# Optimization experiments

Hardware: AMD Instinct MI355X
Metric: run time of the kernel (lower is better)

The kernel has to match this reference:

```python
import jax, jax.numpy as jnp
import numpy as np
from jax import lax

H = 32      # n_heads
D = 128     # head_dim
HID = 4096  # hidden_dim
CQ, CK, CH = 4, 9, 2
G = H // CH  # conv groups == groupnorm groups == 16


def setup_inputs() -> dict:
    key = jax.random.key(0)
    ks = jax.random.split(key, 8)
    q_seqlen = np.array([512, 384, 384, 256], dtype=np.int64)
    kv_seqlen = np.array([512, 384, 384, 256], dtype=np.int64)
    Sq = int(q_seqlen.sum())
    Sk = int(kv_seqlen.sum())
    x = jax.random.normal(ks[0], (Sq, HID), dtype=jnp.float32) * 0.02
    context = jax.random.normal(ks[1], (Sk, HID), dtype=jnp.float32) * 0.02
    wq = jax.random.normal(ks[2], (HID, H * D), dtype=jnp.float32) * 0.02
    wkv = jax.random.normal(ks[3], (HID, 2 * H * D), dtype=jnp.float32) * 0.02
    wo = jax.random.normal(ks[4], (H * D, HID), dtype=jnp.float32) * 0.02
    # grouped conv kernel [out=H, in_per_group=CH, CQ, CK]; dirac-like identity + noise
    conv_w = jax.random.normal(ks[5], (H, CH, CQ, CK), dtype=jnp.float32) * 0.05
    conv_w = conv_w.at[jnp.arange(H), jnp.arange(H) % CH, CQ // 2, CK // 2].add(1.0)
    gn_w = jnp.ones((H,), dtype=jnp.float32)
    gn_b = jnp.zeros((H,), dtype=jnp.float32)
    return {"x": x, "context": context, "wq": wq, "wkv": wkv, "wo": wo,
            "conv_w": conv_w, "gn_w": gn_w, "gn_b": gn_b,
            "q_seqlen": q_seqlen, "kv_seqlen": kv_seqlen}


def _block_diag_mask(q_seqlen, kv_seqlen, dtype):
    # block-diagonal ones mask for packed ragged sequences (static lengths)
    q_len = np.asarray(q_seqlen)
    k_len = np.asarray(kv_seqlen)
    seg_q = np.repeat(np.arange(len(q_len)), q_len)
    seg_k = np.repeat(np.arange(len(k_len)), k_len)
    return jnp.asarray(seg_q[:, None] == seg_k[None, :], dtype=dtype)


def reference(x, context, wq, wkv, wo, conv_w, gn_w, gn_b, q_seqlen, kv_seqlen):
    S = x.shape[0]
    mask = _block_diag_mask(q_seqlen, kv_seqlen, x.dtype)  # [Sq, Sk]
    scale = 1.0 / np.sqrt(D).astype(np.float32)
    q = (x @ wq).reshape(S, H, D).transpose(1, 0, 2) * scale        # [H, Sq, D]
    kv = context @ wkv
    k = kv[:, : H * D].reshape(-1, H, D).transpose(1, 0, 2)         # [H, Sk, D]
    v = kv[:, H * D :].reshape(-1, H, D).transpose(1, 0, 2)         # [H, Sk, D]
    attn = jnp.einsum('hqd,hkd->hqk', q, k) * mask[None]            # [H, Sq, Sk]
    # grouped Conv2d over (query, key) positions, channels = heads
    a = lax.conv_general_dilated(
        attn[None], conv_w, window_strides=(1, 1),
        padding=((CQ // 2, CQ // 2), (CK // 2, CK // 2)),
        dimension_numbers=('NCHW', 'OIHW', 'NCHW'),
        feature_group_count=G)[0]                                   # [H, Sq+1, Sk]
    a = a[:, :-1, :]  # c_q even -> drop extra row (c_k odd -> no col drop)
    a = jax.nn.softmax(a + mask[None], axis=-1)                     # note: +1 bias inside blocks, not -inf
    out = jnp.einsum('hqk,hkd->hqd', a, v)                          # [H, Sq, D]
    # GroupNorm(num_groups=G, channels=H) over [1, H, Sq, D]
    og = out.reshape(G, CH, S, D)
    mu = og.mean(axis=(1, 2, 3), keepdims=True)
    var = og.var(axis=(1, 2, 3), keepdims=True)
    og = (og - mu) * lax.rsqrt(var + 1e-5)
    out = og.reshape(H, S, D) * gn_w[:, None, None] + gn_b[:, None, None]
    out = out.transpose(1, 0, 2).reshape(S, H * D)
    return out @ wo
```

## Files before the change

kernel.cpp:

```cpp
#include <hip/hip_runtime.h>
#include <stdint.h>


#define H_   32
#define D_   128
#define HID_ 4096
#define WMAX2 944
#define LPAD 8

typedef unsigned short bfr;
typedef __attribute__((ext_vector_type(4))) float f32x4;
typedef __attribute__((ext_vector_type(4))) int   i32x4;
typedef __attribute__((ext_vector_type(8))) unsigned short u16x8;
typedef __attribute__((ext_vector_type(4))) unsigned short u16x4;

__device__ __forceinline__ bfr f2bf(float f) {
  uint32_t u = __float_as_uint(f);
  u += 0x7fffu + ((u >> 16) & 1u);
  return (bfr)(u >> 16);
}
__device__ __forceinline__ float bf2f(bfr u) {
  return __uint_as_float(((uint32_t)u) << 16);
}
__device__ __forceinline__ void mfma_bf16(f32x4& d, i32x4 a, i32x4 b) {
// ... 63 lines not shown

__global__ __launch_bounds__(256) void transpose_cvt(
    const float* __restrict__ in, bfr* __restrict__ out, int R, int ld)
{
  __shared__ float tile[64][65];
  const int t = threadIdx.x;
  const int rb = blockIdx.y * 64, cb = blockIdx.x * 64;
  const int row = t >> 2, c4 = (t & 3) * 16;
  const float* gp = in + (long long)(rb + row) * ld + cb + c4;
  #pragma unroll
  for (int j = 0; j < 4; ++j) {
    f32x4 v = *(const f32x4*)(gp + j * 4);
    #pragma unroll
    for (int q = 0; q < 4; ++q) tile[row][c4 + j * 4 + q] = v[q];
  }
  __syncthreads();
  const int cc = row, r4 = c4;
  u16x8 a, b;
  #pragma unroll
  for (int j = 0; j < 8; ++j) a[j] = f2bf(tile[r4 + j][cc]);
  #pragma unroll
  for (int j = 0; j < 8; ++j) b[j] = f2bf(tile[r4 + 8 + j][cc]);
  bfr* op = out + (long long)(cb + cc) * R + rb + r4;
  *(u16x8*)op = a;
  *(u16x8*)(op + 8) = b;
}

__global__ __launch_bounds__(256) void transpose_b16(
    const bfr* __restrict__ in, bfr* __restrict__ out, int R, int C)
{
  __shared__ bfr t[64][72];
  const int z = blockIdx.z;
  const bfr* ip = in + (long long)z * R * C;
  bfr* op = out + (long long)z * R * C;
  const int rb = blockIdx.y * 64, cb = blockIdx.x * 64;
  const int tr = threadIdx.x >> 3;
  const int tc = (threadIdx.x & 7) * 8;
  #pragma unroll
  for (int half = 0; half < 2; ++half) {
    const int r = tr + half * 32;
    u16x8 v = *(const u16x8*)(ip + (long long)(rb + r) * C + cb + tc);
    *(u16x8*)&t[r][tc] = v;
  }
  __syncthreads();
  #pragma unroll
  for (int half = 0; half < 2; ++half) {
    const int cc = tr + half * 32;
    u16x8 vv;
    #pragma unroll
    for (int j = 0; j < 8; ++j) vv[j] = t[tc + j][cc];
    *(u16x8*)(op + (long long)(cb + cc) * R + rb + tc) = vv;
  }
}

__global__ __launch_bounds__(256) void colsum_v(
    const bfr* __restrict__ vt, float* __restrict__ cs, int Sk)
{
  const int lane = threadIdx.x & 63, wave = threadIdx.x >> 6;
  const int row = blockIdx.x * 4 + wave;
  const bfr* src = vt + (long long)row * Sk;
  float s = 0.f;
  for (int i = lane * 8; i + 8 <= Sk; i += 512) {
    u16x8 v = *(const u16x8*)(src + i);
    #pragma unroll
    for (int j = 0; j < 8; ++j) s += bf2f(v[j]);
  }
  #pragma unroll
  for (int m = 1; m < 64; m <<= 1) s += __shfl_xor(s, m);
  if (lane == 0) cs[row] = s;
}

struct GemmAux {
  const int* segq; const int* segk; const int* bk;
  bfr* qb; bfr* kb; bfr* vrow;
  float* outb; float* stats;
  const float* fvArr; const float* colsum;
  float scale;
  int S, Sk, nOff;
};

enum { MODE_PLAIN = 0, MODE_Q = 1, MODE_KV = 2, MODE_QK = 3, MODE_PV = 4 };

template <int MODE, int KS = 1>
__global__ __launch_bounds__(256) void gemm_bt(
    const bfr* __restrict__ A, const bfr* __restrict__ Bt, void* __restrict__ Cout,
    int N, int K, int lda, int ldb,
    long long aZ, long long bZ, long long cZ, GemmAux aux)
{
  __shared__ bfr As[128 * 32];
  __shared__ bfr Bs[128 * 32];
  __shared__ float redS[8], redSS[8];
  const int tid = threadIdx.x;
  const int lane = tid & 63;
  const int wave = tid >> 6;
  const int z = blockIdx.z;

  int bx = blockIdx.x, by = blockIdx.y;
  {
    const int gx = gridDim.x, gy = gridDim.y;
    if (((gx & 3) == 0) && ((gy & 1) == 0)) {
      const int lid = by * gx + bx;
      const int xcd = lid & 7, inner = lid >> 3;
      const int cm = gy >> 1, cn = gx >> 2;
      by = (xcd >> 2) * cm + inner / cn;
      bx = (xcd & 3) * cn + inner % cn;
    }
  }
  const int m0 = by * 128;
  const int n0 = bx * 128;
  const bfr* Ap = A + (long long)z * aZ;
  const bfr* Bp = Bt + (long long)z * bZ;

  if constexpr (MODE == MODE_QK) {
    const int t127 = min(m0 + 127, aux.S - 1);
    const int loT = max(aux.bk[aux.segq[max(m0 - 2, 0)]] - 4, 0);
    const int hiT = min(aux.bk[aux.segq[min(t127 + 1, aux.S - 1)] + 1] + 4, aux.Sk);
    if (n0 > hiT + 16 || n0 + 127 < loT - 16) return;
    const int sm0 = aux.segq[m0], sm1 = aux.segq[t127];
    const int sn0 = aux.segk[n0], sn1 = aux.segk[min(n0 + 127, aux.Sk - 1)];
    if (sm1 < sn0 || sn1 < sm0) {
      bfr* C = (bfr*)Cout + (long long)z * cZ + (long long)m0 * aux.Sk + n0;
      const i32x4 zz = {0, 0, 0, 0};
      #pragma unroll
      for (int c = 0; c < 8; ++c) {
        int id = c * 256 + tid;
        int r = id >> 4, col = (id & 15) * 8;
        *(i32x4*)(C + (long long)r * aux.Sk + col) = zz;
      }
      return;
    }
  }

  int kLo = 0, kHiV = K;
  if constexpr (KS > 1) {
    const int kspan = K / KS;
    kLo = z * kspan;
    kHiV = kLo + kspan;
  }
  if constexpr (MODE == MODE_PV) {
    const int t127 = min(m0 + 127, aux.S - 1);
    kLo = (max(aux.bk[aux.segq[max(m0 - 2, 0)]] - 4, 0)) & ~31;
    int th = min(aux.bk[aux.segq[min(t127 + 1, aux.S - 1)] + 1] + 4, aux.Sk);
    kHiV = min((th + 31) & ~31, aux.Sk);
  }

  const int wr = (wave >> 1) * 64;
  const int wc = (wave & 1) * 64;
  f32x4 acc[4][4];
  #pragma unroll
  for (int i = 0; i < 4; ++i)
    #pragma unroll
    for (int j = 0; j < 4; ++j) acc[i][j] = (f32x4){0.f, 0.f, 0.f, 0.f};

  const int srow = lane >> 2;
  const int scol = (((lane & 3) ^ ((lane >> 2) & 3)) << 3);
  const int rcol = (((lane >> 4) ^ (lane & 3)) << 3);

  const int kSteps = (kHiV - kLo) >> 5;
  for (int ks = 0; ks < kSteps; ++ks) {
    const int k0 = kLo + (ks << 5);
    #pragma unroll
    for (int c = 0; c < 4; ++c) {
      const int chunk = (wave << 2) + c;
      const int ci = chunk & 7;
      const int row = ci * 16 + srow;
      if (chunk < 8) gload_lds16(Ap + (long long)(m0 + row) * lda + k0 + scol, As + ci * 512);
      else           gload_lds16(Bp + (long long)(n0 + row) * ldb + k0 + scol, Bs + ci * 512);
    }
    __syncthreads();
    i32x4 af[4], bfv[4];
    #pragma unroll
    for (int i = 0; i < 4; ++i)
      af[i] = *(const i32x4*)&As[(wr + i * 16 + (lane & 15)) * 32 + rcol];
    #pragma unroll
    for (int i = 0; i < 4; ++i)
      bfv[i] = *(const i32x4*)&Bs[(wc + i * 16 + (lane & 15)) * 32 + rcol];
    #pragma unroll
    for (int i = 0; i < 4; ++i)
      #pragma unroll
      for (int j = 0; j < 4; ++j)
        mfma_bf16(acc[i][j], af[i], bfv[j]);
    __syncthreads();
  }

  bool qkUni = false;
  int sgm[16], sgn[4];
  float fvm[16], csn[4];
  if constexpr (MODE == MODE_QK) {
    const int sA = aux.segq[m0], sB = aux.segq[min(m0 + 127, aux.S - 1)];
    const int sC = aux.segk[n0], sD = aux.segk[min(n0 + 127, aux.Sk - 1)];
    qkUni = (sA == sB) && (sC == sD);
    if (!qkUni) {
      #pragma unroll
      for (int i = 0; i < 4; ++i)
        #pragma unroll
        for (int r = 0; r < 4; ++r)
          sgm[i * 4 + r] = aux.segq[m0 + wr + i * 16 + (lane >> 4) * 4 + r];
      #pragma unroll
      for (int j = 0; j < 4; ++j) sgn[j] = aux.segk[n0 + wc + j * 16 + (lane & 15)];
    }
  }
  if constexpr (MODE == MODE_PV) {
    #pragma unroll
    for (int i = 0; i < 4; ++i)
      #pragma unroll
      for (int r = 0; r < 4; ++r)
        fvm[i * 4 + r] = aux.fvArr[(long long)z * aux.S + m0 + wr + i * 16 + (lane >> 4) * 4 + r];
    #pragma unroll
    for (int j = 0; j < 4; ++j)
      csn[j] = aux.colsum[(long long)z * D_ + n0 + wc + j * 16 + (lane & 15)];
  }

  float sv = 0.f, sq2 = 0.f;
  #pragma unroll
  for (int i = 0; i < 4; ++i) {
    #pragma unroll
    for (int j = 0; j < 4; ++j) {
      #pragma unroll
      for (int r = 0; r < 4; ++r) {
        const int m = m0 + wr + i * 16 + (lane >> 4) * 4 + r;
        const int n = n0 + wc + j * 16 + (lane & 15);
        const float v = acc[i][j][r];
        if constexpr (KS > 1) {
          aux.outb[((long long)z * aux.S + m) * N + n] = v;
        } else if constexpr (MODE == MODE_PLAIN) {
          ((float*)Cout)[(long long)m * N + n] = v;
        } else if constexpr (MODE == MODE_Q) {
          const int hh = n >> 7, d = n & 127;
          aux.qb[((long long)hh * aux.S + m) * D_ + d] = f2bf(v * aux.scale);
        } else if constexpr (MODE == MODE_KV) {
          const int ng = n + aux.nOff;
          if (ng < H_ * D_) {
            const int hh = ng >> 7, d = ng & 127;
            aux.kb[((long long)hh * aux.Sk + m) * D_ + d] = f2bf(v);
          } else {
            const int nv = ng - H_ * D_;
            const int hh = nv >> 7, d = nv & 127;
            aux.vrow[((long long)hh * aux.Sk + m) * D_ + d] = f2bf(v);
          }
        } else if constexpr (MODE == MODE_QK) {
          const float vv = (qkUni || sgm[i * 4 + r] == sgn[j]) ? v : 0.f;
          ((bfr*)Cout)[(long long)z * cZ + (long long)m * aux.Sk + n] = f2bf(vv);
        } else if constexpr (MODE == MODE_PV) {
          const float vv = v + fvm[i * 4 + r] * csn[j];
          aux.outb[((long long)z * aux.S + m) * D_ + n] = vv;
          sv += vv; sq2 += vv * vv;
        }
      }
    }
  }

  if constexpr (MODE == MODE_PV && KS == 1) {
    #pragma unroll
    for (int msk = 1; msk < 64; msk <<= 1) {
      sv  += __shfl_xor(sv, msk);
      sq2 += __shfl_xor(sq2, msk);
    }
    if (lane == 0) { redS[wave] = sv; redSS[wave] = sq2; }
    __syncthreads();
    if (tid == 0) {
      const float a = redS[0] + redS[1] + redS[2] + redS[3];
      const float b = redSS[0] + redSS[1] + redSS[2] + redSS[3];
      atomicAdd(&aux.stats[(z >> 1) * 2 + 0], a);
      atomicAdd(&aux.stats[(z >> 1) * 2 + 1], b);
    }
  }
}

__global__ __launch_bounds__(256) void reduce_split_q(
    const float* __restrict__ part, bfr* __restrict__ qb, float scale, int S)
{
  const long long MN = (long long)S * HID_;
  const long long i = ((long long)blockIdx.x * 256 + threadIdx.x) * 8;
  if (i >= MN) return;
  const f32x4 a0 = *(const f32x4*)(part + i);
  const f32x4 a1 = *(const f32x4*)(part + i + 4);
  const f32x4 b0 = *(const f32x4*)(part + MN + i);
  const f32x4 b1 = *(const f32x4*)(part + MN + i + 4);
  const int m = (int)(i >> 12);
  const int n = (int)(i & 4095);
  const int hh = n >> 7, d = n & 127;
  u16x8 o;
  #pragma unroll
  for (int j = 0; j < 4; ++j) {
    o[j]     = f2bf((a0[j] + b0[j]) * scale);
    o[4 + j] = f2bf((a1[j] + b1[j]) * scale);
  }
  *(u16x8*)(qb + ((long long)hh * S + m) * D_ + d) = o;
}

__global__ __launch_bounds__(256) void reduce_split_f32(
    const float* __restrict__ part, float* __restrict__ out, long long MN)
{
  const long long i = ((long long)blockIdx.x * 256 + threadIdx.x) * 8;
  if (i >= MN) return;
  const f32x4 a0 = *(const f32x4*)(part + i);
  const f32x4 a1 = *(const f32x4*)(part + i + 4);
  const f32x4 b0 = *(const f32x4*)(part + MN + i);
  const f32x4 b1 = *(const f32x4*)(part + MN + i + 4);
  f32x4 o0, o1;
  #pragma unroll
  for (int j = 0; j < 4; ++j) { o0[j] = a0[j] + b0[j]; o1[j] = a1[j] + b1[j]; }
  *(f32x4*)(out + i) = o0;
  *(f32x4*)(out + i + 4) = o1;
}

__global__ __launch_bounds__(256) void conv_softmax4(
    const bfr* __restrict__ attn, const float* __restrict__ conv_w,
    bfr* __restrict__ p, float* __restrict__ fvArr,
    const int* __restrict__ segq, const int* __restrict__ segk,
    const int* __restrict__ bk, int S, int Sk, int h0)
{
  __shared__ float wsh[144];
  __shared__ bfr sIn[7][WMAX2];
  const int tid = threadIdx.x, lane = tid & 63, w = tid >> 6;
  const int q0 = blockIdx.x * 4;
  const int c0 = blockIdx.y * 2;
  const int h  = h0 + c0;
  if (tid < 144) wsh[tid] = conv_w[h * 72 + tid];

  const int lo0 = (max(bk[segq[max(q0 - 2, 0)]] - 4, 0)) & ~7;
  const int hiL = min(bk[segq[min(q0 + 4, S - 1)] + 1] + 4, Sk);
  const int g0 = max(lo0 - 8, 0) & ~7;
  const int g1 = min(hiL + 4, Sk);
  const int W8 = (g1 - g0 + 7) >> 3;

  const int qa = q0 + w;
  const int loA = (max(bk[segq[max(qa - 2, 0)]] - 4, 0)) & ~7;
  const int hiA = min(bk[segq[min(qa + 1, S - 1)] + 1] + 4, Sk);
  const int sqA = segq[qa];
  const int width = hiA - loA;

  float lg[2][4][4];
  #pragma unroll
  for (int e = 0; e < 2; ++e)
    #pragma unroll
    for (int pp = 0; pp < 4; ++pp)
      #pragma unroll
      for (int o = 0; o < 4; ++o) lg[e][pp][o] = 0.f;

  if (tid < 7) {
    const u16x8 zz8 = {0,0,0,0,0,0,0,0};
    *(u16x8*)&sIn[tid][0] = zz8;
    *(u16x8*)&sIn[tid][LPAD + W8 * 8] = zz8;
  }

  for (int pass = 0; pass < 2; ++pass) {
    if (pass) __syncthreads();
    const bfr* src0 = attn + (long long)(c0 + pass) * S * Sk;
    for (int it = tid; it < 7 * 116; it += 256) {
      const int ri = it / 116;
      const int j  = it - ri * 116;
      if (j < W8) {
        const int r = q0 - 2 + ri;
        u16x8 v = {0,0,0,0,0,0,0,0};
        if (r >= 0 && r < S) v = *(const u16x8*)(src0 + (long long)r * Sk + g0 + j * 8);
        *(u16x8*)&sIn[ri][LPAD + j * 8] = v;
      }
    }
    __syncthreads();

    #pragma unroll
    for (int pp = 0; pp < 4; ++pp) {
      const int kk = loA + pp * 256 + lane * 4;
      if (kk < hiA) {
        const int ib = LPAD + kk - 4 - g0;
        #pragma unroll
        for (int rr = 0; rr < 4; ++rr) {
          const bfr* sp = &sIn[w + rr][ib];
          u16x4 u0 = *(const u16x4*)(sp);
          u16x4 u1 = *(const u16x4*)(sp + 4);
          u16x4 u2 = *(const u16x4*)(sp + 8);
          float xx[12];
          #pragma unroll
          for (int j2 = 0; j2 < 4; ++j2) {
            xx[j2]     = bf2f(u0[j2]);
            xx[4 + j2] = bf2f(u1[j2]);
            xx[8 + j2] = bf2f(u2[j2]);
          }
          const float* wv0 = &wsh[(pass * 4 + rr) * 9];
          const float* wv1 = wv0 + 72;
          #pragma unroll
          for (int dk = 0; dk < 9; ++dk) {
            #pragma unroll
            for (int o = 0; o < 4; ++o) {
              lg[0][pp][o] += xx[o + dk] * wv0[dk];
              lg[1][pp][o] += xx[o + dk] * wv1[dk];
            }
          }
        }
      }
    }
  }

  float lmax0 = -1e30f, lmax1 = -1e30f;
  #pragma unroll
  for (int pp = 0; pp < 4; ++pp) {
    const int kk = loA + pp * 256 + lane * 4;
    i32x4 sk4 = {0, 0, 0, 0};
    if (kk < Sk) sk4 = *(const i32x4*)&segk[kk];
    #pragma unroll
    for (int o = 0; o < 4; ++o) {
      const int k = kk + o;
      float v0 = -1e30f, v1 = -1e30f;
      if (k < hiA) {
        const float mb = (sk4[o] == sqA) ? 1.f : 0.f;
        v0 = lg[0][pp][o] + mb; lmax0 = fmaxf(lmax0, v0);
        v1 = lg[1][pp][o] + mb; lmax1 = fmaxf(lmax1, v1);
      }
      lg[0][pp][o] = v0; lg[1][pp][o] = v1;
    }
  }
  #pragma unroll
  for (int m = 1; m < 64; m <<= 1) {
    lmax0 = fmaxf(lmax0, __shfl_xor(lmax0, m));
    lmax1 = fmaxf(lmax1, __shfl_xor(lmax1, m));
  }
  const float M0 = fmaxf(lmax0, 0.f), M1 = fmaxf(lmax1, 0.f);
  float ls0 = 0.f, ls1 = 0.f;
  #pragma unroll
  for (int pp = 0; pp < 4; ++pp)
    #pragma unroll
    for (int o = 0; o < 4; ++o) {
      const float e0 = __expf(lg[0][pp][o] - M0);
      const float e1 = __expf(lg[1][pp][o] - M1);
      lg[0][pp][o] = e0; ls0 += e0;
      lg[1][pp][o] = e1; ls1 += e1;
    }
  #pragma unroll
  for (int m = 1; m < 64; m <<= 1) {
    ls0 += __shfl_xor(ls0, m);
    ls1 += __shfl_xor(ls1, m);
  }
// ... 80 lines not shown
                              void* d_out, int out_size, void* d_ws, size_t ws_size,
                              hipStream_t stream)
{
  const float* x      = (const float*)d_in[0];
  const float* ctx    = (const float*)d_in[1];
  const float* wq     = (const float*)d_in[2];
  const float* wkv    = (const float*)d_in[3];
  const float* wo     = (const float*)d_in[4];
  const float* conv_w = (const float*)d_in[5];
  const float* gnw    = (const float*)d_in[6];
  const float* gnb    = (const float*)d_in[7];
  const void*  qsl    = d_in[8];
  const void*  ksl    = d_in[9];
  const int S    = in_sizes[0] / HID_;
  const int Sk   = in_sizes[1] / HID_;
  const int nseg = in_sizes[8];

  auto al = [](size_t v) { return (v + 255) & ~(size_t)255; };
  char* base = (char*)d_ws;
  size_t off = 0;
  auto take = [&](size_t bytes) -> char* { char* r = base + off; off += al(bytes); return r; };

  int*   segq  = (int*)take((size_t)S * 4);
  int*   segk  = (int*)take((size_t)Sk * 4);
  int*   bq    = (int*)take(64);
  int*   bk    = (int*)take(64);
  float* stats = (float*)take(128);
  float* mr    = (float*)take(128);
  float* fvArr = (float*)take((size_t)H_ * S * 4);
  float* csV   = (float*)take((size_t)H_ * D_ * 4);
  bfr*   qb    = (bfr*)take((size_t)H_ * S * D_ * 2);
  bfr*   kbuf  = (bfr*)take((size_t)H_ * Sk * D_ * 2);
  bfr*   vrow  = (bfr*)take((size_t)H_ * Sk * D_ * 2);
  bfr*   vt    = (bfr*)take((size_t)H_ * Sk * D_ * 2);
  float* outb  = (float*)take((size_t)H_ * S * D_ * 4);
  const size_t poolBase = off;
  char*  pool  = base + poolBase;

  const int Smax = (S > Sk) ? S : Sk;
  const size_t A1 = al((size_t)Smax * HID_ * 2);
  const size_t WT = al((size_t)HID_ * HID_ * 2);
  const size_t PART = al((size_t)2 * S * HID_ * 4);

  const size_t CAmin = al((size_t)4 * S * Sk * 2);
  const size_t fusedNeed = (A1 + 2 * WT > 2 * CAmin) ? (A1 + 2 * WT) : (2 * CAmin);
  const bool fused = (poolBase + fusedNeed <= ws_size);
  const bool splitOK = (poolBase + A1 + 2 * WT + PART <= ws_size);
  const size_t wNeed = A1 + (fused ? 2 : 1) * WT + (splitOK ? PART : 0);

  int nc = 4;
  {
    const int cands[3] = {32, 16, 8};
    for (int ci = 0; ci < 3; ++ci) {
      const size_t CA = al((size_t)cands[ci] * S * Sk * 2);
      const size_t need = (wNeed > 2 * CA) ? wNeed : (2 * CA);
      if (poolBase + need <= ws_size) { nc = cands[ci]; break; }
    }
  }
  const size_t CA = al((size_t)nc * S * Sk * 2);
  bfr*   xcb    = (bfr*)pool;
  bfr*   wT     = (bfr*)(pool + A1);
  float* partB  = (float*)(pool + A1 + 2 * WT);
  bfr*   attn_c = (bfr*)pool;
  bfr*   pbuf_c = (bfr*)(pool + CA);

  seg_setup<<<1, 256, 0, stream>>>(qsl, ksl, segq, segk, bq, bk, stats, S, Sk, nseg);

  GemmAux aux{};
  aux.segq = segq; aux.segk = segk; aux.bk = bk;
  aux.qb = qb; aux.kb = kbuf; aux.vrow = vrow;
  aux.outb = outb; aux.stats = stats;
  aux.fvArr = fvArr; aux.colsum = csV;
  aux.scale = 0.08838834764831845f;
  aux.S = S; aux.Sk = Sk; aux.nOff = 0;

  const long long MN = (long long)S * HID_;
  const int nRed = (int)((MN / 8 + 255) / 256);

  const long long nx = (long long)S * HID_;
  cvt_bf16<<<(int)((nx / 8 + 255) / 256), 256, 0, stream>>>(x, xcb, nx);
  transpose_cvt<<<dim3(HID_ / 64, HID_ / 64), 256, 0, stream>>>(wq, wT, HID_, HID_);
  if (splitOK) {
    GemmAux auxQ = aux; auxQ.outb = partB;
    gemm_bt<MODE_Q, 2><<<dim3(HID_ / 128, S / 128, 2), 256, 0, stream>>>(
        xcb, wT, nullptr, HID_, HID_, HID_, HID_, 0, 0, 0, auxQ);
    reduce_split_q<<<nRed, 256, 0, stream>>>(partB, qb, aux.scale, S);
  } else {
    gemm_bt<MODE_Q><<<dim3(HID_ / 128, S / 128, 1), 256, 0, stream>>>(
        xcb, wT, nullptr, HID_, HID_, HID_, HID_, 0, 0, 0, aux);
  }

  const long long nctx = (long long)Sk * HID_;
  cvt_bf16<<<(int)((nctx / 8 + 255) / 256), 256, 0, stream>>>(ctx, xcb, nctx);
  if (fused) {
    transpose_cvt<<<dim3(2 * HID_ / 64, HID_ / 64), 256, 0, stream>>>(wkv, wT, HID_, 2 * HID_);
    gemm_bt<MODE_KV><<<dim3(2 * HID_ / 128, Sk / 128, 1), 256, 0, stream>>>(
        xcb, wT, nullptr, 2 * HID_, HID_, HID_, HID_, 0, 0, 0, aux);
  } else {
    transpose_cvt<<<dim3(HID_ / 64, HID_ / 64), 256, 0, stream>>>(wkv, wT, HID_, 2 * HID_);
    gemm_bt<MODE_KV><<<dim3(HID_ / 128, Sk / 128, 1), 256, 0, stream>>>(
        xcb, wT, nullptr, HID_, HID_, HID_, HID_, 0, 0, 0, aux);
    transpose_cvt<<<dim3(HID_ / 64, HID_ / 64), 256, 0, stream>>>(wkv + HID_, wT, HID_, 2 * HID_);
    GemmAux auxV = aux; auxV.nOff = H_ * D_;
    gemm_bt<MODE_KV><<<dim3(HID_ / 128, Sk / 128, 1), 256, 0, stream>>>(
        xcb, wT, nullptr, HID_, HID_, HID_, HID_, 0, 0, 0, auxV);
  }

  transpose_b16<<<dim3(D_ / 64, Sk / 64, H_), 256, 0, stream>>>(vrow, vt, Sk, D_);
  colsum_v<<<H_ * D_ / 4, 256, 0, stream>>>(vt, csV, Sk);

  for (int h0 = 0; h0 < H_; h0 += nc) {
    gemm_bt<MODE_QK><<<dim3(Sk / 128, S / 128, nc), 256, 0, stream>>>(
        qb + (size_t)h0 * S * D_, kbuf + (size_t)h0 * Sk * D_, attn_c,
        Sk, D_, D_, D_,
        (long long)S * D_, (long long)Sk * D_, (long long)S * Sk, aux);
    conv_softmax4<<<dim3(S / 4, nc / 2), 256, 0, stream>>>(
        attn_c, conv_w, pbuf_c, fvArr, segq, segk, bk, S, Sk, h0);
    GemmAux auxP = aux;
    auxP.outb = outb + (size_t)h0 * S * D_;
    auxP.stats = stats + h0;
    auxP.fvArr = fvArr + (size_t)h0 * S;
    auxP.colsum = csV + (size_t)h0 * D_;
    gemm_bt<MODE_PV><<<dim3(1, S / 128, nc), 256, 0, stream>>>(
        pbuf_c, vt + (size_t)h0 * D_ * Sk, nullptr,
        D_, Sk, Sk, Sk,
        (long long)S * Sk, (long long)D_ * Sk, 0, auxP);
  }

  gn_finalize<<<1, 32, 0, stream>>>(stats, mr, 1.0f / (2.0f * S * D_));
  gn_apply<<<dim3((S * D_) / 2048, H_), 256, 0, stream>>>(outb, mr, gnw, gnb, xcb, S);
  transpose_cvt<<<dim3(HID_ / 64, HID_ / 64), 256, 0, stream>>>(wo, wT, HID_, HID_);
  if (splitOK) {
    GemmAux auxO = aux; auxO.outb = partB;
    gemm_bt<MODE_PLAIN, 2><<<dim3(HID_ / 128, S / 128, 2), 256, 0, stream>>>(
        xcb, wT, nullptr, HID_, HID_, HID_, HID_, 0, 0, 0, auxO);
    reduce_split_f32<<<nRed, 256, 0, stream>>>(partB, (float*)d_out, MN);
  } else {
    gemm_bt<MODE_PLAIN><<<dim3(HID_ / 128, S / 128, 1), 256, 0, stream>>>(
        xcb, wT, d_out, HID_, HID_, HID_, HID_, 0, 0, 0, aux);
  }
}
```

Baseline: 544.0 us.

## Add double-buffered 512-thread GEMM for projections and widen conv-softmax blocks

Adds a new gemm_bt8 kernel with 8 waves, a BK=64 tile and double-buffered LDS staging. It prefetches the next k-tile with async global-to-LDS loads while MFMAs run on the current one, and is used for the Q, KV and output projection GEMMs. The QK/PV GEMM keeps the old kernel but loses its XOR swizzle, which may bring back LDS bank conflicts. The conv-softmax kernel now processes 8 query rows per 512-thread block instead of 4, reusing more of the staged halo rows. The larger LDS footprint (64KB for the GEMM) lowers occupancy.

```diff
diff --git a/kernel.cpp b/kernel.cpp
--- a/kernel.cpp
+++ b/kernel.cpp
@@ -169,14 +169,12 @@
 enum { MODE_PLAIN = 0, MODE_Q = 1, MODE_KV = 2, MODE_QK = 3, MODE_PV = 4 };
 
 template <int MODE, int KS = 1>
-__global__ __launch_bounds__(256) void gemm_bt(
+__global__ __launch_bounds__(512) void gemm_bt8(
     const bfr* __restrict__ A, const bfr* __restrict__ Bt, void* __restrict__ Cout,
-    int N, int K, int lda, int ldb,
-    long long aZ, long long bZ, long long cZ, GemmAux aux)
-{
-  __shared__ bfr As[128 * 32];
-  __shared__ bfr Bs[128 * 32];
-  __shared__ float redS[8], redSS[8];
+    int N, int K, int lda, int ldb, GemmAux aux)
+{
+  __shared__ bfr As[2][128 * 64];
+  __shared__ bfr Bs[2][128 * 64];
   const int tid = threadIdx.x;
   const int lane = tid & 63;
   const int wave = tid >> 6;
@@ -193,116 +191,69 @@
       bx = (xcd & 3) * cn + inner % cn;
     }
   }
-  const int m0 = by * 128;
-  const int n0 = bx * 128;
-  const bfr* Ap = A + (long long)z * aZ;
-  const bfr* Bp = Bt + (long long)z * bZ;
-
-  if constexpr (MODE == MODE_QK) {
-    const int t127 = min(m0 + 127, aux.S - 1);
-    const int loT = max(aux.bk[aux.segq[max(m0 - 2, 0)]] - 4, 0);
-    const int hiT = min(aux.bk[aux.segq[min(t127 + 1, aux.S - 1)] + 1] + 4, aux.Sk);
-    if (n0 > hiT + 16 || n0 + 127 < loT - 16) return;
-    const int sm0 = aux.segq[m0], sm1 = aux.segq[t127];
-    const int sn0 = aux.segk[n0], sn1 = aux.segk[min(n0 + 127, aux.Sk - 1)];
-    if (sm1 < sn0 || sn1 < sm0) {
-      bfr* C = (bfr*)Cout + (long long)z * cZ + (long long)m0 * aux.Sk + n0;
-      const i32x4 zz = {0, 0, 0, 0};
-      #pragma unroll
-      for (int c = 0; c < 8; ++c) {
-        int id = c * 256 + tid;
-        int r = id >> 4, col = (id & 15) * 8;
-        *(i32x4*)(C + (long long)r * aux.Sk + col) = zz;
-      }
-      return;
-    }
-  }
-
-  int kLo = 0, kHiV = K;
-  if constexpr (KS > 1) {
-    const int kspan = K / KS;
-    kLo = z * kspan;
-    kHiV = kLo + kspan;
-  }
-  if constexpr (MODE == MODE_PV) {
-    const int t127 = min(m0 + 127, aux.S - 1);
-    kLo = (max(aux.bk[aux.segq[max(m0 - 2, 0)]] - 4, 0)) & ~31;
-    int th = min(aux.bk[aux.segq[min(t127 + 1, aux.S - 1)] + 1] + 4, aux.Sk);
-    kHiV = min((th + 31) & ~31, aux.Sk);
-  }
-
-  const int wr = (wave >> 1) * 64;
-  const int wc = (wave & 1) * 64;
-  f32x4 acc[4][4];
+  const int m0 = by * 128, n0 = bx * 128;
+
+  int kLo = 0, kHi = K;
+  if constexpr (KS > 1) { const int ksp = K / KS; kLo = z * ksp; kHi = kLo + ksp; }
+
+  const int wr = (wave >> 2) * 64;
+  const int wc = (wave & 3) * 32;
+  f32x4 acc[4][2];
   #pragma unroll
   for (int i = 0; i < 4; ++i)
     #pragma unroll
-    for (int j = 0; j < 4; ++j) acc[i][j] = (f32x4){0.f, 0.f, 0.f, 0.f};
-
-  const int srow = lane >> 2;
-  const int scol = (((lane & 3) ^ ((lane >> 2) & 3)) << 3);
-  const int rcol = (((lane >> 4) ^ (lane & 3)) << 3);
-
-  const int kSteps = (kHiV - kLo) >> 5;
-  for (int ks = 0; ks < kSteps; ++ks) {
-    const int k0 = kLo + (ks << 5);
+    for (int j = 0; j < 2; ++j) acc[i][j] = (f32x4){0.f, 0.f, 0.f, 0.f};
+
+  const int srow8 = lane >> 3;
+  const int scol  = (lane & 7) * 8;
+  auto STAGE = [&](int k0, int b) {
     #pragma unroll
     for (int c = 0; c < 4; ++c) {
       const int chunk = (wave << 2) + c;
-      const int ci = chunk & 7;
-      const int row = ci * 16 + srow;
-      if (chunk < 8) gload_lds16(Ap + (long long)(m0 + row) * lda + k0 + scol, As + ci * 512);
-      else           gload_lds16(Bp + (long long)(n0 + row) * ldb + k0 + scol, Bs + ci * 512);
-    }
-    __syncthreads();
-    i32x4 af[4], bfv[4];
-    #pragma unroll
-    for (int i = 0; i < 4; ++i)
-      af[i] = *(const i32x4*)&As[(wr + i * 16 + (lane & 15)) * 32 + rcol];
-    #pragma unroll
-    for (int i = 0; i < 4; ++i)
-      bfv[i] = *(const i32x4*)&Bs[(wc + i * 16 + (lane & 15)) * 32 + rcol];
-    #pragma unroll
-    for (int i = 0; i < 4; ++i)
-      #pragma unroll
-      for (int j = 0; j < 4; ++j)
-        mfma_bf16(acc[i][j], af[i], bfv[j]);
-    __syncthreads();
-  }
-
-  bool qkUni = false;
-  int sgm[16], sgn[4];
-  float fvm[16], csn[4];
-  if constexpr (MODE == MODE_QK) {
-    const int sA = aux.segq[m0], sB = aux.segq[min(m0 + 127, aux.S - 1)];
-    const int sC = aux.segk[n0], sD = aux.segk[min(n0 + 127, aux.Sk - 1)];
-    qkUni = (sA == sB) && (sC == sD);
-    if (!qkUni) {
+      const int ci = chunk & 15;
+      const int row = ci * 8 + srow8;
+      if (chunk < 16) gload_lds16(A  + (long long)(m0 + row) * lda + k0 + scol, &As[b][ci * 512]);
+      else            gload_lds16(Bt + (long long)(n0 + row) * ldb + k0 + scol, &Bs[b][ci * 512]);
+    }
+  };
+
+  const int nk = (kHi - kLo) >> 6;
+  STAGE(kLo, 0);
+  int cur = 0;
+  for (int t = 0; t < nk; ++t) {
+    if (t + 1 < nk) {
+      STAGE(kLo + ((t + 1) << 6), cur ^ 1);
+      asm volatile("s_waitcnt vmcnt(4)" ::: "memory");
+    } else {
+      asm volatile("s_waitcnt vmcnt(0)" ::: "memory");
+    }
+    __builtin_amdgcn_s_barrier();
+    __builtin_amdgcn_sched_barrier(0);
+    #pragma unroll
+    for (int ks2 = 0; ks2 < 2; ++ks2) {
+      const int colb = ks2 * 32 + (lane >> 4) * 8;
+      i32x4 af[4], bfv[2];
+      #pragma unroll
+      for (int i = 0; i < 4; ++i)
+        af[i] = *(const i32x4*)&As[cur][(wr + i * 16 + (lane & 15)) * 64 + colb];
+      #pragma unroll
+      for (int j = 0; j < 2; ++j)
+        bfv[j] = *(const i32x4*)&Bs[cur][(wc + j * 16 + (lane & 15)) * 64 + colb];
       #pragma unroll
       for (int i = 0; i < 4; ++i)
         #pragma unroll
-        for (int r = 0; r < 4; ++r)
-          sgm[i * 4 + r] = aux.segq[m0 + wr + i * 16 + (lane >> 4) * 4 + r];
-      #pragma unroll
-      for (int j = 0; j < 4; ++j) sgn[j] = aux.segk[n0 + wc + j * 16 + (lane & 15)];
-    }
-  }
-  if constexpr (MODE == MODE_PV) {
-    #pragma unroll
-    for (int i = 0; i < 4; ++i)
-      #pragma unroll
-      for (int r = 0; r < 4; ++r)
-        fvm[i * 4 + r] = aux.fvArr[(long long)z * aux.S + m0 + wr + i * 16 + (lane >> 4) * 4 + r];
-    #pragma unroll
-    for (int j = 0; j < 4; ++j)
-      csn[j] = aux.colsum[(long long)z * D_ + n0 + wc + j * 16 + (lane & 15)];
-  }
-
-  float sv = 0.f, sq2 = 0.f;
+        for (int j = 0; j < 2; ++j)
+          mfma_bf16(acc[i][j], af[i], bfv[j]);
+    }
+    __builtin_amdgcn_sched_barrier(0);
+    __builtin_amdgcn_s_barrier();
+    cur ^= 1;
+  }
+
   #pragma unroll
   for (int i = 0; i < 4; ++i) {
     #pragma unroll
-    for (int j = 0; j < 4; ++j) {
+    for (int j = 0; j < 2; ++j) {
       #pragma unroll
       for (int r = 0; r < 4; ++r) {
         const int m = m0 + wr + i * 16 + (lane >> 4) * 4 + r;
@@ -325,7 +276,145 @@
             const int hh = nv >> 7, d = nv & 127;
             aux.vrow[((long long)hh * aux.Sk + m) * D_ + d] = f2bf(v);
           }
-        } else if constexpr (MODE == MODE_QK) {
+        }
+      }
+    }
+  }
+}
+
+template <int MODE>
+__global__ __launch_bounds__(256) void gemm_bt(
+    const bfr* __restrict__ A, const bfr* __restrict__ Bt, void* __restrict__ Cout,
+    int N, int K, int lda, int ldb,
+    long long aZ, long long bZ, long long cZ, GemmAux aux)
+{
+  __shared__ bfr As[128 * 32];
+  __shared__ bfr Bs[128 * 32];
+  __shared__ float redS[8], redSS[8];
+  const int tid = threadIdx.x;
+  const int lane = tid & 63;
+  const int wave = tid >> 6;
+  const int z = blockIdx.z;
+
+  int bx = blockIdx.x, by = blockIdx.y;
+  {
+    const int gx = gridDim.x, gy = gridDim.y;
+    if (((gx & 3) == 0) && ((gy & 1) == 0)) {
+      const int lid = by * gx + bx;
+      const int xcd = lid & 7, inner = lid >> 3;
+      const int cm = gy >> 1, cn = gx >> 2;
+      by = (xcd >> 2) * cm + inner / cn;
+      bx = (xcd & 3) * cn + inner % cn;
+    }
+  }
+  const int m0 = by * 128;
+  const int n0 = bx * 128;
+  const bfr* Ap = A + (long long)z * aZ;
+  const bfr* Bp = Bt + (long long)z * bZ;
+
+  if constexpr (MODE == MODE_QK) {
+    const int t127 = min(m0 + 127, aux.S - 1);
+    const int loT = max(aux.bk[aux.segq[max(m0 - 2, 0)]] - 4, 0);
+    const int hiT = min(aux.bk[aux.segq[min(t127 + 1, aux.S - 1)] + 1] + 4, aux.Sk);
+    if (n0 > hiT + 16 || n0 + 127 < loT - 16) return;
+    const int sm0 = aux.segq[m0], sm1 = aux.segq[t127];
+    const int sn0 = aux.segk[n0], sn1 = aux.segk[min(n0 + 127, aux.Sk - 1)];
+    if (sm1 < sn0 || sn1 < sm0) {
+      bfr* C = (bfr*)Cout + (long long)z * cZ + (long long)m0 * aux.Sk + n0;
+      const i32x4 zz = {0, 0, 0, 0};
+      #pragma unroll
+      for (int c = 0; c < 8; ++c) {
+        int id = c * 256 + tid;
+        int r = id >> 4, col = (id & 15) * 8;
+        *(i32x4*)(C + (long long)r * aux.Sk + col) = zz;
+      }
+      return;
+    }
+  }
+
+  int kLo = 0, kHiV = K;
+  if constexpr (MODE == MODE_PV) {
+    const int t127 = min(m0 + 127, aux.S - 1);
+    kLo = (max(aux.bk[aux.segq[max(m0 - 2, 0)]] - 4, 0)) & ~31;
+    int th = min(aux.bk[aux.segq[min(t127 + 1, aux.S - 1)] + 1] + 4, aux.Sk);
+    kHiV = min((th + 31) & ~31, aux.Sk);
+  }
+
+  const int wr = (wave >> 1) * 64;
+  const int wc = (wave & 1) * 64;
+  f32x4 acc[4][4];
+  #pragma unroll
+  for (int i = 0; i < 4; ++i)
+    #pragma unroll
+    for (int j = 0; j < 4; ++j) acc[i][j] = (f32x4){0.f, 0.f, 0.f, 0.f};
+
+  const int kSteps = (kHiV - kLo) >> 5;
+  for (int ks = 0; ks < kSteps; ++ks) {
+    const int k0 = kLo + (ks << 5);
+    #pragma unroll
+    for (int c = 0; c < 4; ++c) {
+      const int chunk = (wave << 2) + c;
+      const int ci = chunk & 7;
+      const int row = ci * 16 + (lane >> 2);
+      const int col = (lane & 3) * 8;
+      if (chunk < 8) gload_lds16(Ap + (long long)(m0 + row) * lda + k0 + col, As + ci * 512);
+      else           gload_lds16(Bp + (long long)(n0 + row) * ldb + k0 + col, Bs + ci * 512);
+    }
+    __syncthreads();
+    i32x4 af[4], bfv[4];
+    #pragma unroll
+    for (int i = 0; i < 4; ++i)
+      af[i] = *(const i32x4*)&As[(wr + i * 16 + (lane & 15)) * 32 + (lane >> 4) * 8];
+    #pragma unroll
+    for (int i = 0; i < 4; ++i)
+      bfv[i] = *(const i32x4*)&Bs[(wc + i * 16 + (lane & 15)) * 32 + (lane >> 4) * 8];
+    #pragma unroll
+    for (int i = 0; i < 4; ++i)
+      #pragma unroll
+      for (int j = 0; j < 4; ++j)
+        mfma_bf16(acc[i][j], af[i], bfv[j]);
+    __syncthreads();
+  }
+
+  bool qkUni = false;
+  int sgm[16], sgn[4];
+  float fvm[16], csn[4];
+  if constexpr (MODE == MODE_QK) {
+    const int sA = aux.segq[m0], sB = aux.segq[min(m0 + 127, aux.S - 1)];
+    const int sC = aux.segk[n0], sD = aux.segk[min(n0 + 127, aux.Sk - 1)];
+    qkUni = (sA == sB) && (sC == sD);
+    if (!qkUni) {
+      #pragma unroll
+      for (int i = 0; i < 4; ++i)
+        #pragma unroll
+        for (int r = 0; r < 4; ++r)
+          sgm[i * 4 + r] = aux.segq[m0 + wr + i * 16 + (lane >> 4) * 4 + r];
+      #pragma unroll
+      for (int j = 0; j < 4; ++j) sgn[j] = aux.segk[n0 + wc + j * 16 + (lane & 15)];
+    }
+  }
+  if constexpr (MODE == MODE_PV) {
+    #pragma unroll
+    for (int i = 0; i < 4; ++i)
+      #pragma unroll
+      for (int r = 0; r < 4; ++r)
+        fvm[i * 4 + r] = aux.fvArr[(long long)z * aux.S + m0 + wr + i * 16 + (lane >> 4) * 4 + r];
+    #pragma unroll
+    for (int j = 0; j < 4; ++j)
+      csn[j] = aux.colsum[(long long)z * D_ + n0 + wc + j * 16 + (lane & 15)];
+  }
+
+  float sv = 0.f, sq2 = 0.f;
+  #pragma unroll
+  for (int i = 0; i < 4; ++i) {
+    #pragma unroll
+    for (int j = 0; j < 4; ++j) {
+      #pragma unroll
+      for (int r = 0; r < 4; ++r) {
+        const int m = m0 + wr + i * 16 + (lane >> 4) * 4 + r;
+        const int n = n0 + wc + j * 16 + (lane & 15);
+        const float v = acc[i][j][r];
+        if constexpr (MODE == MODE_QK) {
           const float vv = (qkUni || sgm[i * 4 + r] == sgn[j]) ? v : 0.f;
           ((bfr*)Cout)[(long long)z * cZ + (long long)m * aux.Sk + n] = f2bf(vv);
         } else if constexpr (MODE == MODE_PV) {
@@ -337,7 +426,7 @@
     }
   }
 
-  if constexpr (MODE == MODE_PV && KS == 1) {
+  if constexpr (MODE == MODE_PV) {
     #pragma unroll
     for (int msk = 1; msk < 64; msk <<= 1) {
       sv  += __shfl_xor(sv, msk);
@@ -392,22 +481,22 @@
   *(f32x4*)(out + i + 4) = o1;
 }
 
-__global__ __launch_bounds__(256) void conv_softmax4(
+__global__ __launch_bounds__(512) void conv_softmax5(
     const bfr* __restrict__ attn, const float* __restrict__ conv_w,
     bfr* __restrict__ p, float* __restrict__ fvArr,
     const int* __restrict__ segq, const int* __restrict__ segk,
     const int* __restrict__ bk, int S, int Sk, int h0)
 {
   __shared__ float wsh[144];
-  __shared__ bfr sIn[7][WMAX2];
+  __shared__ bfr sIn[11][WMAX2];
   const int tid = threadIdx.x, lane = tid & 63, w = tid >> 6;
-  const int q0 = blockIdx.x * 4;
+  const int q0 = blockIdx.x * 8;
   const int c0 = blockIdx.y * 2;
   const int h  = h0 + c0;
   if (tid < 144) wsh[tid] = conv_w[h * 72 + tid];
 
   const int lo0 = (max(bk[segq[max(q0 - 2, 0)]] - 4, 0)) & ~7;
-  const int hiL = min(bk[segq[min(q0 + 4, S - 1)] + 1] + 4, Sk);
+  const int hiL = min(bk[segq[min(q0 + 8, S - 1)] + 1] + 4, Sk);
   const int g0 = max(lo0 - 8, 0) & ~7;
   const int g1 = min(hiL + 4, Sk);
   const int W8 = (g1 - g0 + 7) >> 3;
@@ -426,7 +515,7 @@
       #pragma unroll
       for (int o = 0; o < 4; ++o) lg[e][pp][o] = 0.f;
 
-  if (tid < 7) {
+  if (tid < 11) {
     const u16x8 zz8 = {0,0,0,0,0,0,0,0};
     *(u16x8*)&sIn[tid][0] = zz8;
     *(u16x8*)&sIn[tid][LPAD + W8 * 8] = zz8;
@@ -435,7 +524,7 @@
   for (int pass = 0; pass < 2; ++pass) {
     if (pass) __syncthreads();
     const bfr* src0 = attn + (long long)(c0 + pass) * S * Sk;
-    for (int it = tid; it < 7 * 116; it += 256) {
+    for (int it = tid; it < 11 * 116; it += 512) {
       const int ri = it / 116;
       const int j  = it - ri * 116;
       if (j < W8) {
@@ -682,28 +771,28 @@
   transpose_cvt<<<dim3(HID_ / 64, HID_ / 64), 256, 0, stream>>>(wq, wT, HID_, HID_);
   if (splitOK) {
     GemmAux auxQ = aux; auxQ.outb = partB;
-    gemm_bt<MODE_Q, 2><<<dim3(HID_ / 128, S / 128, 2), 256, 0, stream>>>(
-        xcb, wT, nullptr, HID_, HID_, HID_, HID_, 0, 0, 0, auxQ);
+    gemm_bt8<MODE_Q, 2><<<dim3(HID_ / 128, S / 128, 2), 512, 0, stream>>>(
+        xcb, wT, nullptr, HID_, HID_, HID_, HID_, auxQ);
     reduce_split_q<<<nRed, 256, 0, stream>>>(partB, qb, aux.scale, S);
   } else {
-    gemm_bt<MODE_Q><<<dim3(HID_ / 128, S / 128, 1), 256, 0, stream>>>(
-        xcb, wT, nullptr, HID_, HID_, HID_, HID_, 0, 0, 0, aux);
+    gemm_bt8<MODE_Q><<<dim3(HID_ / 128, S / 128, 1), 512, 0, stream>>>(
+        xcb, wT, nullptr, HID_, HID_, HID_, HID_, aux);
   }
 
   const long long nctx = (long long)Sk * HID_;
   cvt_bf16<<<(int)((nctx / 8 + 255) / 256), 256, 0, stream>>>(ctx, xcb, nctx);
   if (fused) {
     transpose_cvt<<<dim3(2 * HID_ / 64, HID_ / 64), 256, 0, stream>>>(wkv, wT, HID_, 2 * HID_);
-    gemm_bt<MODE_KV><<<dim3(2 * HID_ / 128, Sk / 128, 1), 256, 0, stream>>>(
-        xcb, wT, nullptr, 2 * HID_, HID_, HID_, HID_, 0, 0, 0, aux);
+    gemm_bt8<MODE_KV><<<dim3(2 * HID_ / 128, Sk / 128, 1), 512, 0, stream>>>(
+        xcb, wT, nullptr, 2 * HID_, HID_, HID_, HID_, aux);
   } else {
     transpose_cvt<<<dim3(HID_ / 64, HID_ / 64), 256, 0, stream>>>(wkv, wT, HID_, 2 * HID_);
-    gemm_bt<MODE_KV><<<dim3(HID_ / 128, Sk / 128, 1), 256, 0, stream>>>(
-        xcb, wT, nullptr, HID_, HID_, HID_, HID_, 0, 0, 0, aux);
+    gemm_bt8<MODE_KV><<<dim3(HID_ / 128, Sk / 128, 1), 512, 0, stream>>>(
+        xcb, wT, nullptr, HID_, HID_, HID_, HID_, aux);
     transpose_cvt<<<dim3(HID_ / 64, HID_ / 64), 256, 0, stream>>>(wkv + HID_, wT, HID_, 2 * HID_);
     GemmAux auxV = aux; auxV.nOff = H_ * D_;
-    gemm_bt<MODE_KV><<<dim3(HID_ / 128, Sk / 128, 1), 256, 0, stream>>>(
-        xcb, wT, nullptr, HID_, HID_, HID_, HID_, 0, 0, 0, auxV);
+    gemm_bt8<MODE_KV><<<dim3(HID_ / 128, Sk / 128, 1), 512, 0, stream>>>(
+        xcb, wT, nullptr, HID_, HID_, HID_, HID_, auxV);
   }
 
   transpose_b16<<<dim3(D_ / 64, Sk / 64, H_), 256, 0, stream>>>(vrow, vt, Sk, D_);
@@ -714,7 +803,7 @@
         qb + (size_t)h0 * S * D_, kbuf + (size_t)h0 * Sk * D_, attn_c,
         Sk, D_, D_, D_,
         (long long)S * D_, (long long)Sk * D_, (long long)S * Sk, aux);
-    conv_softmax4<<<dim3(S / 4, nc / 2), 256, 0, stream>>>(
+    conv_softmax5<<<dim3(S / 8, nc / 2), 512, 0, stream>>>(
         attn_c, conv_w, pbuf_c, fvArr, segq, segk, bk, S, Sk, h0);
     GemmAux auxP = aux;
     auxP.outb = outb + (size_t)h0 * S * D_;
@@ -732,11 +821,11 @@
   transpose_cvt<<<dim3(HID_ / 64, HID_ / 64), 256, 0, stream>>>(wo, wT, HID_, HID_);
   if (splitOK) {
     GemmAux auxO = aux; auxO.outb = partB;
-    gemm_bt<MODE_PLAIN, 2><<<dim3(HID_ / 128, S / 128, 2), 256, 0, stream>>>(
-        xcb, wT, nullptr, HID_, HID_, HID_, HID_, 0, 0, 0, auxO);
+    gemm_bt8<MODE_PLAIN, 2><<<dim3(HID_ / 128, S / 128, 2), 512, 0, stream>>>(
+        xcb, wT, nullptr, HID_, HID_, HID_, HID_, auxO);
     reduce_split_f32<<<nRed, 256, 0, stream>>>(partB, (float*)d_out, MN);
   } else {
-    gemm_bt<MODE_PLAIN><<<dim3(HID_ / 128, S / 128, 1), 256, 0, stream>>>(
-        xcb, wT, d_out, HID_, HID_, HID_, HID_, 0, 0, 0, aux);
-  }
-}
+    gemm_bt8<MODE_PLAIN><<<dim3(HID_ / 128, S / 128, 1), 512, 0, stream>>>(
+        xcb, wT, d_out, HID_, HID_, HID_, HID_, aux);
+  }
+}
```

After: 635.3 us. +16.8%, slower.

## Add dedicated single-shot QK GEMM kernel and widen conv-softmax blocks to 8 rows

Applied to the files above, without the earlier changes.

Moves the QK^T score GEMM into its own kernel that loads the full K=128 depth of both 128x128 tiles into LDS at once and runs four MFMA k-steps with a single barrier, instead of looping over 32-wide k-chunks with two barriers per chunk. The XCD tile remapping is dropped for this kernel. The conv+softmax kernel now handles 8 query rows per block with 512 threads and an 11-row halo instead of 4 rows and 7, which cuts redundant halo loads. The trade-off is 64KB of LDS per QK block, which lowers occupancy, and higher register and LDS pressure in the softmax kernel.

```diff
diff --git a/kernel.cpp b/kernel.cpp
--- a/kernel.cpp
+++ b/kernel.cpp
@@ -198,32 +198,8 @@
   const bfr* Ap = A + (long long)z * aZ;
   const bfr* Bp = Bt + (long long)z * bZ;
 
-  if constexpr (MODE == MODE_QK) {
-    const int t127 = min(m0 + 127, aux.S - 1);
-    const int loT = max(aux.bk[aux.segq[max(m0 - 2, 0)]] - 4, 0);
-    const int hiT = min(aux.bk[aux.segq[min(t127 + 1, aux.S - 1)] + 1] + 4, aux.Sk);
-    if (n0 > hiT + 16 || n0 + 127 < loT - 16) return;
-    const int sm0 = aux.segq[m0], sm1 = aux.segq[t127];
-    const int sn0 = aux.segk[n0], sn1 = aux.segk[min(n0 + 127, aux.Sk - 1)];
-    if (sm1 < sn0 || sn1 < sm0) {
-      bfr* C = (bfr*)Cout + (long long)z * cZ + (long long)m0 * aux.Sk + n0;
-      const i32x4 zz = {0, 0, 0, 0};
-      #pragma unroll
-      for (int c = 0; c < 8; ++c) {
-        int id = c * 256 + tid;
-        int r = id >> 4, col = (id & 15) * 8;
-        *(i32x4*)(C + (long long)r * aux.Sk + col) = zz;
-      }
-      return;
-    }
-  }
-
   int kLo = 0, kHiV = K;
-  if constexpr (KS > 1) {
-    const int kspan = K / KS;
-    kLo = z * kspan;
-    kHiV = kLo + kspan;
-  }
+  if constexpr (KS > 1) { const int ksp = K / KS; kLo = z * ksp; kHiV = kLo + ksp; }
   if constexpr (MODE == MODE_PV) {
     const int t127 = min(m0 + 127, aux.S - 1);
     kLo = (max(aux.bk[aux.segq[max(m0 - 2, 0)]] - 4, 0)) & ~31;
@@ -270,23 +246,7 @@
     __syncthreads();
   }
 
-  bool qkUni = false;
-  int sgm[16], sgn[4];
   float fvm[16], csn[4];
-  if constexpr (MODE == MODE_QK) {
-    const int sA = aux.segq[m0], sB = aux.segq[min(m0 + 127, aux.S - 1)];
-    const int sC = aux.segk[n0], sD = aux.segk[min(n0 + 127, aux.Sk - 1)];
-    qkUni = (sA == sB) && (sC == sD);
-    if (!qkUni) {
-      #pragma unroll
-      for (int i = 0; i < 4; ++i)
-        #pragma unroll
-        for (int r = 0; r < 4; ++r)
-          sgm[i * 4 + r] = aux.segq[m0 + wr + i * 16 + (lane >> 4) * 4 + r];
-      #pragma unroll
-      for (int j = 0; j < 4; ++j) sgn[j] = aux.segk[n0 + wc + j * 16 + (lane & 15)];
-    }
-  }
   if constexpr (MODE == MODE_PV) {
     #pragma unroll
     for (int i = 0; i < 4; ++i)
@@ -325,9 +285,6 @@
             const int hh = nv >> 7, d = nv & 127;
             aux.vrow[((long long)hh * aux.Sk + m) * D_ + d] = f2bf(v);
           }
-        } else if constexpr (MODE == MODE_QK) {
-          const float vv = (qkUni || sgm[i * 4 + r] == sgn[j]) ? v : 0.f;
-          ((bfr*)Cout)[(long long)z * cZ + (long long)m * aux.Sk + n] = f2bf(vv);
         } else if constexpr (MODE == MODE_PV) {
           const float vv = v + fvm[i * 4 + r] * csn[j];
           aux.outb[((long long)z * aux.S + m) * D_ + n] = vv;
@@ -350,6 +307,107 @@
       const float b = redSS[0] + redSS[1] + redSS[2] + redSS[3];
       atomicAdd(&aux.stats[(z >> 1) * 2 + 0], a);
       atomicAdd(&aux.stats[(z >> 1) * 2 + 1], b);
+    }
+  }
+}
+
+__global__ __launch_bounds__(256) void gemm_qk(
+    const bfr* __restrict__ A, const bfr* __restrict__ Bt, bfr* __restrict__ Cout,
+    long long aZ, long long bZ, long long cZ, GemmAux aux)
+{
+  __shared__ bfr As[128 * 128];
+  __shared__ bfr Bs[128 * 128];
+  const int tid = threadIdx.x;
+  const int lane = tid & 63;
+  const int wave = tid >> 6;
+  const int z = blockIdx.z;
+  const int m0 = blockIdx.y * 128;
+  const int n0 = blockIdx.x * 128;
+
+  const int t127 = min(m0 + 127, aux.S - 1);
+  const int loT = max(aux.bk[aux.segq[max(m0 - 2, 0)]] - 4, 0);
+  const int hiT = min(aux.bk[aux.segq[min(t127 + 1, aux.S - 1)] + 1] + 4, aux.Sk);
+  if (n0 > hiT + 16 || n0 + 127 < loT - 16) return;
+  const int sm0 = aux.segq[m0], sm1 = aux.segq[t127];
+  const int sn0 = aux.segk[n0], sn1 = aux.segk[min(n0 + 127, aux.Sk - 1)];
+  if (sm1 < sn0 || sn1 < sm0) {
+    bfr* C = Cout + (long long)z * cZ + (long long)m0 * aux.Sk + n0;
+    const i32x4 zz = {0, 0, 0, 0};
+    #pragma unroll
+    for (int c = 0; c < 8; ++c) {
+      int id = c * 256 + tid;
+      int r = id >> 4, col = (id & 15) * 8;
+      *(i32x4*)(C + (long long)r * aux.Sk + col) = zz;
+    }
+    return;
+  }
+
+  const bfr* Ap = A + (long long)z * aZ;
+  const bfr* Bp = Bt + (long long)z * bZ;
+
+  const int srow = lane >> 4;
+  const int scol = (lane & 15) * 8;
+  #pragma unroll
+  for (int c = 0; c < 16; ++c) {
+    const int chunk = wave * 16 + c;
+    if (chunk < 32) {
+      const int r = chunk * 4 + srow;
+      gload_lds16(Ap + (long long)(m0 + r) * D_ + scol, As + chunk * 512);
+    } else {
+      const int r = (chunk - 32) * 4 + srow;
+      gload_lds16(Bp + (long long)(n0 + r) * D_ + scol, Bs + (chunk - 32) * 512);
+    }
+  }
+  __syncthreads();
+
+  const int wr = (wave >> 1) * 64;
+  const int wc = (wave & 1) * 64;
+  f32x4 acc[4][4];
+  #pragma unroll
+  for (int i = 0; i < 4; ++i)
+    #pragma unroll
+    for (int j = 0; j < 4; ++j) acc[i][j] = (f32x4){0.f, 0.f, 0.f, 0.f};
+
+  #pragma unroll
+  for (int ks = 0; ks < 4; ++ks) {
+    const int colb = ks * 32 + (lane >> 4) * 8;
+    i32x4 af[4], bfv[4];
+    #pragma unroll
+    for (int i = 0; i < 4; ++i)
+      af[i] = *(const i32x4*)&As[(wr + i * 16 + (lane & 15)) * 128 + colb];
+    #pragma unroll
+    for (int j = 0; j < 4; ++j)
+      bfv[j] = *(const i32x4*)&Bs[(wc + j * 16 + (lane & 15)) * 128 + colb];
+    #pragma unroll
+    for (int i = 0; i < 4; ++i)
+      #pragma unroll
+      for (int j = 0; j < 4; ++j)
+        mfma_bf16(acc[i][j], af[i], bfv[j]);
+  }
+
+  const bool qkUni = (sm0 == sm1) && (sn0 == sn1);
+  int sgm[16], sgn[4];
+  if (!qkUni) {
+    #pragma unroll
+    for (int i = 0; i < 4; ++i)
+      #pragma unroll
+      for (int r = 0; r < 4; ++r)
+        sgm[i * 4 + r] = aux.segq[m0 + wr + i * 16 + (lane >> 4) * 4 + r];
+    #pragma unroll
+    for (int j = 0; j < 4; ++j) sgn[j] = aux.segk[n0 + wc + j * 16 + (lane & 15)];
+  }
+  #pragma unroll
+  for (int i = 0; i < 4; ++i) {
+    #pragma unroll
+    for (int j = 0; j < 4; ++j) {
+      #pragma unroll
+      for (int r = 0; r < 4; ++r) {
+        const int m = m0 + wr + i * 16 + (lane >> 4) * 4 + r;
+        const int n = n0 + wc + j * 16 + (lane & 15);
+        const float v = acc[i][j][r];
+        const float vv = (qkUni || sgm[i * 4 + r] == sgn[j]) ? v : 0.f;
+        Cout[(long long)z * cZ + (long long)m * aux.Sk + n] = f2bf(vv);
+      }
     }
   }
 }
@@ -392,22 +450,22 @@
   *(f32x4*)(out + i + 4) = o1;
 }
 
-__global__ __launch_bounds__(256) void conv_softmax4(
+__global__ __launch_bounds__(512) void conv_softmax5(
     const bfr* __restrict__ attn, const float* __restrict__ conv_w,
     bfr* __restrict__ p, float* __restrict__ fvArr,
     const int* __restrict__ segq, const int* __restrict__ segk,
     const int* __restrict__ bk, int S, int Sk, int h0)
 {
   __shared__ float wsh[144];
-  __shared__ bfr sIn[7][WMAX2];
+  __shared__ bfr sIn[11][WMAX2];
   const int tid = threadIdx.x, lane = tid & 63, w = tid >> 6;
-  const int q0 = blockIdx.x * 4;
+  const int q0 = blockIdx.x * 8;
   const int c0 = blockIdx.y * 2;
   const int h  = h0 + c0;
   if (tid < 144) wsh[tid] = conv_w[h * 72 + tid];
 
   const int lo0 = (max(bk[segq[max(q0 - 2, 0)]] - 4, 0)) & ~7;
-  const int hiL = min(bk[segq[min(q0 + 4, S - 1)] + 1] + 4, Sk);
+  const int hiL = min(bk[segq[min(q0 + 8, S - 1)] + 1] + 4, Sk);
   const int g0 = max(lo0 - 8, 0) & ~7;
   const int g1 = min(hiL + 4, Sk);
   const int W8 = (g1 - g0 + 7) >> 3;
@@ -426,7 +484,7 @@
       #pragma unroll
       for (int o = 0; o < 4; ++o) lg[e][pp][o] = 0.f;
 
-  if (tid < 7) {
+  if (tid < 11) {
     const u16x8 zz8 = {0,0,0,0,0,0,0,0};
     *(u16x8*)&sIn[tid][0] = zz8;
     *(u16x8*)&sIn[tid][LPAD + W8 * 8] = zz8;
@@ -435,7 +493,7 @@
   for (int pass = 0; pass < 2; ++pass) {
     if (pass) __syncthreads();
     const bfr* src0 = attn + (long long)(c0 + pass) * S * Sk;
-    for (int it = tid; it < 7 * 116; it += 256) {
+    for (int it = tid; it < 11 * 116; it += 512) {
       const int ri = it / 116;
       const int j  = it - ri * 116;
       if (j < W8) {
@@ -710,11 +768,10 @@
   colsum_v<<<H_ * D_ / 4, 256, 0, stream>>>(vt, csV, Sk);
 
   for (int h0 = 0; h0 < H_; h0 += nc) {
-    gemm_bt<MODE_QK><<<dim3(Sk / 128, S / 128, nc), 256, 0, stream>>>(
+    gemm_qk<<<dim3(Sk / 128, S / 128, nc), 256, 0, stream>>>(
         qb + (size_t)h0 * S * D_, kbuf + (size_t)h0 * Sk * D_, attn_c,
-        Sk, D_, D_, D_,
         (long long)S * D_, (long long)Sk * D_, (long long)S * Sk, aux);
-    conv_softmax4<<<dim3(S / 4, nc / 2), 256, 0, stream>>>(
+    conv_softmax5<<<dim3(S / 8, nc / 2), 512, 0, stream>>>(
         attn_c, conv_w, pbuf_c, fvArr, segq, segk, bk, S, Sk, h0);
     GemmAux auxP = aux;
     auxP.outb = outb + (size_t)h0 * S * D_;
```

Measured after the change: 540.4 us. No clear change (-0.7%).
